# Kernel optimization log

Hardware: AMD Instinct MI355X
Metric: run time of the kernel (lower is better)

## Reference

```python
import jax, jax.numpy as jnp
import numpy as np

B = 131072    # batch of toy 2D points
H = 256       # effective hidden width (dims[1], = out_dims * group_card)
NB = 8        # n_blocks i-ResBlocks
NMID = 3      # middle layers: dims 2->256->256->256->256->2 => 1 in + 3 mid + 1 out
NPS = 5       # n_power_series terms for log-det trace estimator


def setup_inputs() -> dict:
    key = jax.random.key(0)
    ks = jax.random.split(key, 8)
    # small scales keep each g-net contractive (coeff<1 Lipschitz, as spectral norm would)
    x  = jax.random.normal(ks[0], (B, 2), jnp.float32)
    v  = jax.random.normal(ks[1], (B, 2), jnp.float32)  # Hutchinson probe (n_samples=1)
    Wi = jax.random.normal(ks[2], (NB, 2, H), jnp.float32) * 0.05
    bi = jax.random.normal(ks[3], (NB, H), jnp.float32) * 0.01
    Wm = jax.random.normal(ks[4], (NB, NMID, H, H), jnp.float32) * (0.05 / np.sqrt(H))
    bm = jax.random.normal(ks[5], (NB, NMID, H), jnp.float32) * 0.01
    Wo = jax.random.normal(ks[6], (NB, H, 2), jnp.float32) * (0.05 / np.sqrt(H))
    bo = jax.random.normal(ks[7], (NB, 2), jnp.float32) * 0.01
    return {"x": x, "v": v, "Wi": Wi, "bi": bi, "Wm": Wm, "bm": bm, "Wo": Wo, "bo": bo}


def _g(x, Wi, bi, Wm, bm, Wo, bo):
    # equivariant 3x3 convs on 1x1 spatial maps == channel-mixing linears;
    # build_nnet appends the activation after EVERY conv, including the last.
    h = jax.nn.relu(x @ Wi + bi)
    for j in range(Wm.shape[0]):
        h = jax.nn.relu(h @ Wm[j] + bm[j])
    return jax.nn.relu(h @ Wo + bo)


def _iresblock(x, v, Wi, bi, Wm, bm, Wo, bo):
    gfun = lambda xx: _g(xx, Wi, bi, Wm, bm, Wo, bo)
    gx = gfun(x)
    # log det(I + J_g) ~= sum_{k=1..n} (-1)^{k+1}/k * v^T J_g^k v  (power series, Hutchinson)
    w = v
    logdet = jnp.zeros((x.shape[0], 1), x.dtype)
    for k in range(1, NPS + 1):
        _, w = jax.jvp(gfun, (x,), (w,))          # w <- J_g @ w
        coef = ((-1.0) ** (k + 1)) / k
        logdet = logdet + coef * jnp.sum(w * v, axis=1, keepdims=True)
    return x + gx, logdet


def reference(x, v, Wi, bi, Wm, bm, Wo, bo):
    z = x
    delta_logp = jnp.zeros((x.shape[0], 1), x.dtype)  # SequentialFlow: logpx - logdet per block
    for b in range(NB):
        z, ld = _iresblock(z, v, Wi[b], bi[b], Wm[b], bm[b], Wo[b], bo[b])
        delta_logp = delta_logp - ld
    return z, delta_logp
```

## Files before the change

kernel.cpp:

```cpp
#include <hip/hip_runtime.h>
#include <hip/hip_bf16.h>

#define BATCH 131072
#define H 256
#define NBLK 8
#define NMID 3
#define MS 32
#define RT_N 6
#define NT 256

typedef __attribute__((ext_vector_type(8))) short short8;
typedef __attribute__((ext_vector_type(4))) float f32x4;

__device__ __forceinline__ unsigned pk2(float a, float b) {
    unsigned ua = __float_as_uint(a) + 0x8000u;
    unsigned ub = __float_as_uint(b) + 0x8000u;
    return __builtin_amdgcn_perm(ub, ua, 0x07060302u);
}
__device__ __forceinline__ unsigned short f2bf(float f) {
    return (unsigned short)((__float_as_uint(f) + 0x8000u) >> 16);
}

__global__ void pack_w_kernel(const float* __restrict__ Wm, unsigned short* __restrict__ Wp) {
    int o = blockIdx.x * blockDim.x + threadIdx.x;
    if (o >= NBLK * NMID * 8192) return;
    int lane  = o & 63;
    int T     = (o >> 6) & 15;
    int kk    = (o >> 10) & 7;
    int layer = o >> 13;
    int n  = (T >> 2) * 64 + (lane & 15) * 4 + (T & 3);
    int k0 = kk * 32 + (lane >> 4) * 8;
    const float* src = Wm + (size_t)layer * H * H;
    unsigned int w[4];
    #pragma unroll
    for (int jj = 0; jj < 4; ++jj)
        w[jj] = pk2(src[(size_t)(k0 + 2*jj) * H + n], src[(size_t)(k0 + 2*jj + 1) * H + n]);
    uint4 val; val.x = w[0]; val.y = w[1]; val.z = w[2]; val.w = w[3];
    ((uint4*)Wp)[o] = val;
}

__device__ __forceinline__ void epilogue_write(const f32x4 (&acc)[RT_N][4],
                                               const float* __restrict__ bias,
                                               unsigned short* __restrict__ Xs,
                                               int wave, int lane) {
    const int mcol = lane & 15, quad = lane >> 4;
    const int nb = wave * 64 + mcol * 4;
    const float4 bv = *(const float4*)(bias + nb);
    const int kkx = nb >> 5;
    const int qx  = (nb >> 3) & 3;
    const int jb  = nb & 7;
    #pragma unroll
    for (int g = 0; g < 2; ++g) {
        #pragma unroll
        for (int r = 0; r < 4; ++r) {
            float pre[4], hv[4], ta[4], tb[4];
            pre[0] = acc[g][0][r] + bv.x; pre[1] = acc[g][1][r] + bv.y;
            pre[2] = acc[g][2][r] + bv.z; pre[3] = acc[g][3][r] + bv.w;
            #pragma unroll
            for (int c = 0; c < 4; ++c) {
                bool mk = pre[c] > 0.0f;
                hv[c] = mk ? pre[c]        : 0.0f;
                ta[c] = mk ? acc[2+g][c][r] : 0.0f;
                tb[c] = mk ? acc[4+g][c][r] : 0.0f;
            }
            int rowm = quad * 4 + r;
            int le   = qx * 16 + rowm;
            int scl  = le ^ ((le >> 3) & 7);
            int e0   = (((g * 8 + kkx) * 64 + scl) * 8) + jb;
            uint2 ph; ph.x = pk2(hv[0], hv[1]); ph.y = pk2(hv[2], hv[3]);
            uint2 pa; pa.x = pk2(ta[0], ta[1]); pa.y = pk2(ta[2], ta[3]);
            uint2 pb; pb.x = pk2(tb[0], tb[1]); pb.y = pk2(tb[2], tb[3]);
            *(uint2*)(Xs + e0)          = ph;
            *(uint2*)(Xs + e0 + 8192)   = pa;
            *(uint2*)(Xs + e0 + 16384)  = pb;
        }
    }
}

__global__ __launch_bounds__(NT, 2)
void flow_kernel(const float* __restrict__ x, const float* __restrict__ v,
                 const float* __restrict__ Wi, const float* __restrict__ bi,
                 const float* __restrict__ bm, const float* __restrict__ Wo,
                 const float* __restrict__ bo,
                 const unsigned short* __restrict__ Wp,
                 float* __restrict__ out)
{
    __shared__ uint4 Xl4[RT_N * 8 * 64];
    __shared__ float zbuf[MS * 2];
    __shared__ float vbuf[MS * 2];

    unsigned short* Xs = (unsigned short*)Xl4;

    const int tid  = threadIdx.x;
    const int wave = tid >> 6;
    const int lane = tid & 63;
    const int mcol = lane & 15;
    const int quad = lane >> 4;
    const int s0   = blockIdx.x * MS;
    const int rl   = lane ^ ((lane >> 3) & 7);

    float dlp = 0.0f;
    if (tid < MS) {
        zbuf[tid*2+0] = x[(size_t)(s0+tid)*2+0];
        zbuf[tid*2+1] = x[(size_t)(s0+tid)*2+1];
        vbuf[tid*2+0] = v[(size_t)(s0+tid)*2+0];
        vbuf[tid*2+1] = v[(size_t)(s0+tid)*2+1];
    }
    __syncthreads();

    for (int b = 0; b < NBLK; ++b) {
        #pragma unroll
        for (int cc = 0; cc < 2; ++cc) {
            int c = cc * NT + tid;
            if (c < 384) {
                int rt = c >> 6, cl = c & 63;
                int l = cl ^ ((cl >> 3) & 7);
                int m = l & 15, q = l >> 4;
                int st = rt >> 1;
                uint4 pk = {0u, 0u, 0u, 0u};
                if (q == 0) {
                    if (st == 0) {
                        int s = ((rt & 1) << 4) | m;
                        pk.x = pk2(zbuf[s*2+0], zbuf[s*2+1]);
                    } else if (st == 1) pk.x = 0x00003F80u;
                    else                pk.x = 0x3F800000u;
                }
                Xl4[rt * 512 + cl] = pk;
            }
        }
        __syncthreads();

        const float* Wi0 = Wi + (size_t)b * 2 * H;
        const float* Wi1 = Wi0 + H;
        {
            short8 b0[4];
            #pragma unroll
            for (int ct = 0; ct < 4; ++ct) {
                short8 z = {0,0,0,0,0,0,0,0};
                if (lane < 16) {
                    int n = wave * 64 + lane * 4 + ct;
                    unsigned p = pk2(Wi0[n], Wi1[n]);
                    z[0] = (short)(p & 0xFFFFu);
                    z[1] = (short)(p >> 16);
                }
                b0[ct] = z;
            }
            f32x4 acc[RT_N][4];
            #pragma unroll
            for (int rt = 0; rt < RT_N; ++rt)
                #pragma unroll
                for (int ct = 0; ct < 4; ++ct)
                    acc[rt][ct] = (f32x4){0.f, 0.f, 0.f, 0.f};
            #pragma unroll
            for (int rt = 0; rt < RT_N; ++rt) {
                short8 af = ((const short8*)Xl4)[(rt * 8) * 64 + rl];
                #pragma unroll
                for (int ct = 0; ct < 4; ++ct)
                    acc[rt][ct] = __builtin_amdgcn_mfma_f32_16x16x32_bf16(af, b0[ct], acc[rt][ct], 0, 0, 0);
            }
            __syncthreads();
            epilogue_write(acc, bi + (size_t)b * H, Xs, wave, lane);
            __syncthreads();
        }

        for (int li = 0; li < NMID; ++li) {
            const int layer = b * NMID + li;
            const short8* Bp  = ((const short8*)Wp) + (size_t)layer * 8192;
            const float* bias = bm + (size_t)layer * H;

            f32x4 acc[RT_N][4];
            #pragma unroll
            for (int rt = 0; rt < RT_N; ++rt)
                #pragma unroll
                for (int ct = 0; ct < 4; ++ct)
                    acc[rt][ct] = (f32x4){0.f, 0.f, 0.f, 0.f};

            #pragma unroll
            for (int kk = 0; kk < 8; ++kk) {
                short8 bf[4];
                #pragma unroll
                for (int ct = 0; ct < 4; ++ct)
                    bf[ct] = Bp[(kk*16 + wave*4 + ct)*64 + lane];
                #pragma unroll
                for (int rt = 0; rt < RT_N; ++rt) {
                    short8 af = ((const short8*)Xl4)[(rt*8 + kk)*64 + rl];
                    #pragma unroll
                    for (int ct = 0; ct < 4; ++ct)
                        acc[rt][ct] = __builtin_amdgcn_mfma_f32_16x16x32_bf16(af, bf[ct], acc[rt][ct], 0, 0, 0);
                }
            }
            __syncthreads();
            epilogue_write(acc, bias, Xs, wave, lane);
            __syncthreads();
        }

        const float* Wob = Wo + (size_t)b * H * 2;
        const float* bob = bo + (size_t)b * 2;
        {
            short8 b4[2];
            #pragma unroll
            for (int kki = 0; kki < 2; ++kki) {
                short8 z = {0,0,0,0,0,0,0,0};
                if (mcol < 2) {
                    int kb = (wave * 2 + kki) * 32 + quad * 8;
                    #pragma unroll
                    for (int jj = 0; jj < 4; ++jj) {
                        unsigned p = pk2(Wob[(kb + 2*jj) * 2 + mcol], Wob[(kb + 2*jj + 1) * 2 + mcol]);
                        z[2*jj]   = (short)(p & 0xFFFFu);
                        z[2*jj+1] = (short)(p >> 16);
                    }
                }
                b4[kki] = z;
            }
            f32x4 accL[RT_N];
            #pragma unroll
            for (int rt = 0; rt < RT_N; ++rt) accL[rt] = (f32x4){0.f, 0.f, 0.f, 0.f};
            #pragma unroll
            for (int rt = 0; rt < RT_N; ++rt) {
                short8 a0 = ((const short8*)Xl4)[(rt*8 + wave*2    )*64 + rl];
                accL[rt] = __builtin_amdgcn_mfma_f32_16x16x32_bf16(a0, b4[0], accL[rt], 0, 0, 0);
                short8 a1 = ((const short8*)Xl4)[(rt*8 + wave*2 + 1)*64 + rl];
                accL[rt] = __builtin_amdgcn_mfma_f32_16x16x32_bf16(a1, b4[1], accL[rt], 0, 0, 0);
            }
            __syncthreads();
            float* part = (float*)Xl4;
            if (mcol < 2) {
                #pragma unroll
                for (int rt = 0; rt < RT_N; ++rt)
                    #pragma unroll
                    for (int r = 0; r < 4; ++r)
                        part[((rt*16 + quad*4 + r)*2 + mcol)*4 + wave] = accL[rt][r];
            }
            __syncthreads();
            float* res = part + 768;
            if (tid < 192) {
                float4 p4 = ((const float4*)part)[tid];
                res[tid] = p4.x + p4.y + p4.z + p4.w;
            }
            __syncthreads();
            if (tid < MS) {
                int g = tid >> 4, row = tid & 15;
                int base = (g * 16 + row) * 2;
                float SH0 = res[base], SH1 = res[base + 1];
                float SA0 = res[base + 64], SA1 = res[base + 65];
                float SB0 = res[base + 128], SB1 = res[base + 129];
                float pre0 = SH0 + bob[0], pre1 = SH1 + bob[1];
                bool  m0 = pre0 > 0.f,     m1 = pre1 > 0.f;
                float gx0 = m0 ? pre0 : 0.f, gx1 = m1 ? pre1 : 0.f;
                float J00 = m0 ? SA0 : 0.f;
                float J01 = m0 ? SB0 : 0.f;
                float J10 = m1 ? SA1 : 0.f;
                float J11 = m1 ? SB1 : 0.f;
                float v0 = vbuf[tid*2+0], v1 = vbuf[tid*2+1];
                float w0 = v0, w1 = v1, ld = 0.f;
                const float coef[5] = {1.f, -0.5f, 1.f/3.f, -0.25f, 0.2f};
                #pragma unroll
                for (int k = 0; k < 5; ++k) {
                    float nw0 = fmaf(J00, w0, J01 * w1);
                    float nw1 = fmaf(J10, w0, J11 * w1);
                    w0 = nw0; w1 = nw1;
                    ld = fmaf(coef[k], fmaf(w0, v0, w1 * v1), ld);
                }
                zbuf[tid*2+0] += gx0;
                zbuf[tid*2+1] += gx1;
                dlp -= ld;
            }
        }
        __syncthreads();
    }

    if (tid < MS) {
        out[(size_t)(s0+tid)*2+0] = zbuf[tid*2+0];
        out[(size_t)(s0+tid)*2+1] = zbuf[tid*2+1];
        out[(size_t)2*BATCH + s0 + tid] = dlp;
    }
}

extern "C" void kernel_launch(void* const* d_in, const int* in_sizes, int n_in,
                              void* d_out, int out_size, void* d_ws, size_t ws_size,
                              hipStream_t stream) {
    const float* x  = (const float*)d_in[0];
    const float* v  = (const float*)d_in[1];
    const float* Wi = (const float*)d_in[2];
    const float* bi = (const float*)d_in[3];
    const float* Wm = (const float*)d_in[4];
    const float* bm = (const float*)d_in[5];
    const float* Wo = (const float*)d_in[6];
    const float* bo = (const float*)d_in[7];
    unsigned short* Wp = (unsigned short*)d_ws;

    int nchunks = NBLK * NMID * 8192;
    pack_w_kernel<<<(nchunks + 255) / 256, 256, 0, stream>>>(Wm, Wp);
    flow_kernel<<<BATCH / MS, NT, 0, stream>>>(x, v, Wi, bi, bm, Wo, bo, Wp, (float*)d_out);
}
```

Measured before the change: 1.253 ms.

## Split output columns across eight waves per block instead of four

Doubles the block to 512 threads (8 waves) and has each wave own half as many output column tiles in every layer, which halves the accumulator registers per wave. Launch bounds change to allow 4 blocks per CU, and the middle-layer k-loop unroll drops to 2. The output-layer reduction now sums eight per-wave partials. The aim is more resident waves to hide LDS and global weight-load latency. The cost is that each A fragment loaded from LDS feeds only half as many MFMAs, so LDS traffic per unit of compute doubles, and barriers now span more waves.

```diff
diff --git a/kernel.cpp b/kernel.cpp
--- a/kernel.cpp
+++ b/kernel.cpp
@@ -7,7 +7,7 @@
 #define NMID 3
 #define MS 32
 #define RT_N 6
-#define NT 256
+#define NT 512
 
 typedef __attribute__((ext_vector_type(8))) short short8;
 typedef __attribute__((ext_vector_type(4))) float f32x4;
@@ -16,9 +16,6 @@
     unsigned ua = __float_as_uint(a) + 0x8000u;
     unsigned ub = __float_as_uint(b) + 0x8000u;
     return __builtin_amdgcn_perm(ub, ua, 0x07060302u);
-}
-__device__ __forceinline__ unsigned short f2bf(float f) {
-    return (unsigned short)((__float_as_uint(f) + 0x8000u) >> 16);
 }
 
 __global__ void pack_w_kernel(const float* __restrict__ Wm, unsigned short* __restrict__ Wp) {
@@ -39,45 +36,38 @@
     ((uint4*)Wp)[o] = val;
 }
 
-__device__ __forceinline__ void epilogue_write(const f32x4 (&acc)[RT_N][4],
+__device__ __forceinline__ void epilogue_write(const f32x4 (&acc)[RT_N][2],
                                                const float* __restrict__ bias,
                                                unsigned short* __restrict__ Xs,
                                                int wave, int lane) {
     const int mcol = lane & 15, quad = lane >> 4;
-    const int nb = wave * 64 + mcol * 4;
-    const float4 bv = *(const float4*)(bias + nb);
-    const int kkx = nb >> 5;
-    const int qx  = (nb >> 3) & 3;
-    const int jb  = nb & 7;
+    const int C  = (wave >> 1) * 64 + mcol * 4 + ((wave & 1) << 1);
+    const float b0 = bias[C], b1 = bias[C + 1];
+    const int kkx = C >> 5;
+    const int qx  = (C >> 3) & 3;
+    const int jb  = C & 7;
     #pragma unroll
     for (int g = 0; g < 2; ++g) {
         #pragma unroll
         for (int r = 0; r < 4; ++r) {
-            float pre[4], hv[4], ta[4], tb[4];
-            pre[0] = acc[g][0][r] + bv.x; pre[1] = acc[g][1][r] + bv.y;
-            pre[2] = acc[g][2][r] + bv.z; pre[3] = acc[g][3][r] + bv.w;
-            #pragma unroll
-            for (int c = 0; c < 4; ++c) {
-                bool mk = pre[c] > 0.0f;
-                hv[c] = mk ? pre[c]        : 0.0f;
-                ta[c] = mk ? acc[2+g][c][r] : 0.0f;
-                tb[c] = mk ? acc[4+g][c][r] : 0.0f;
-            }
+            float pre0 = acc[g][0][r] + b0;
+            float pre1 = acc[g][1][r] + b1;
+            bool m0 = pre0 > 0.0f, m1 = pre1 > 0.0f;
+            float h0 = m0 ? pre0 : 0.0f,          h1 = m1 ? pre1 : 0.0f;
+            float a0 = m0 ? acc[2+g][0][r] : 0.0f, a1 = m1 ? acc[2+g][1][r] : 0.0f;
+            float t0 = m0 ? acc[4+g][0][r] : 0.0f, t1 = m1 ? acc[4+g][1][r] : 0.0f;
             int rowm = quad * 4 + r;
             int le   = qx * 16 + rowm;
             int scl  = le ^ ((le >> 3) & 7);
             int e0   = (((g * 8 + kkx) * 64 + scl) * 8) + jb;
-            uint2 ph; ph.x = pk2(hv[0], hv[1]); ph.y = pk2(hv[2], hv[3]);
-            uint2 pa; pa.x = pk2(ta[0], ta[1]); pa.y = pk2(ta[2], ta[3]);
-            uint2 pb; pb.x = pk2(tb[0], tb[1]); pb.y = pk2(tb[2], tb[3]);
-            *(uint2*)(Xs + e0)          = ph;
-            *(uint2*)(Xs + e0 + 8192)   = pa;
-            *(uint2*)(Xs + e0 + 16384)  = pb;
-        }
-    }
-}
-
-__global__ __launch_bounds__(NT, 2)
+            *(unsigned*)(Xs + e0)          = pk2(h0, h1);
+            *(unsigned*)(Xs + e0 + 8192)   = pk2(a0, a1);
+            *(unsigned*)(Xs + e0 + 16384)  = pk2(t0, t1);
+        }
+    }
+}
+
+__global__ __launch_bounds__(NT, 4)
 void flow_kernel(const float* __restrict__ x, const float* __restrict__ v,
                  const float* __restrict__ Wi, const float* __restrict__ bi,
                  const float* __restrict__ bm, const float* __restrict__ Wo,
@@ -109,54 +99,50 @@
     __syncthreads();
 
     for (int b = 0; b < NBLK; ++b) {
-        #pragma unroll
-        for (int cc = 0; cc < 2; ++cc) {
-            int c = cc * NT + tid;
-            if (c < 384) {
-                int rt = c >> 6, cl = c & 63;
-                int l = cl ^ ((cl >> 3) & 7);
-                int m = l & 15, q = l >> 4;
-                int st = rt >> 1;
-                uint4 pk = {0u, 0u, 0u, 0u};
-                if (q == 0) {
-                    if (st == 0) {
-                        int s = ((rt & 1) << 4) | m;
-                        pk.x = pk2(zbuf[s*2+0], zbuf[s*2+1]);
-                    } else if (st == 1) pk.x = 0x00003F80u;
-                    else                pk.x = 0x3F800000u;
-                }
-                Xl4[rt * 512 + cl] = pk;
-            }
+        if (tid < 384) {
+            int rt = tid >> 6, cl = tid & 63;
+            int l = cl ^ ((cl >> 3) & 7);
+            int m = l & 15, q = l >> 4;
+            int st = rt >> 1;
+            uint4 pk = {0u, 0u, 0u, 0u};
+            if (q == 0) {
+                if (st == 0) {
+                    int s = ((rt & 1) << 4) | m;
+                    pk.x = pk2(zbuf[s*2+0], zbuf[s*2+1]);
+                } else if (st == 1) pk.x = 0x00003F80u;
+                else                pk.x = 0x3F800000u;
+            }
+            Xl4[rt * 512 + cl] = pk;
         }
         __syncthreads();
 
         const float* Wi0 = Wi + (size_t)b * 2 * H;
         const float* Wi1 = Wi0 + H;
         {
-            short8 b0[4];
-            #pragma unroll
-            for (int ct = 0; ct < 4; ++ct) {
+            short8 b0f[2];
+            #pragma unroll
+            for (int ct = 0; ct < 2; ++ct) {
                 short8 z = {0,0,0,0,0,0,0,0};
                 if (lane < 16) {
-                    int n = wave * 64 + lane * 4 + ct;
+                    int n = (wave >> 1) * 64 + lane * 4 + ((wave & 1) << 1) + ct;
                     unsigned p = pk2(Wi0[n], Wi1[n]);
                     z[0] = (short)(p & 0xFFFFu);
                     z[1] = (short)(p >> 16);
                 }
-                b0[ct] = z;
-            }
-            f32x4 acc[RT_N][4];
+                b0f[ct] = z;
+            }
+            f32x4 acc[RT_N][2];
             #pragma unroll
             for (int rt = 0; rt < RT_N; ++rt)
                 #pragma unroll
-                for (int ct = 0; ct < 4; ++ct)
+                for (int ct = 0; ct < 2; ++ct)
                     acc[rt][ct] = (f32x4){0.f, 0.f, 0.f, 0.f};
             #pragma unroll
             for (int rt = 0; rt < RT_N; ++rt) {
                 short8 af = ((const short8*)Xl4)[(rt * 8) * 64 + rl];
                 #pragma unroll
-                for (int ct = 0; ct < 4; ++ct)
-                    acc[rt][ct] = __builtin_amdgcn_mfma_f32_16x16x32_bf16(af, b0[ct], acc[rt][ct], 0, 0, 0);
+                for (int ct = 0; ct < 2; ++ct)
+                    acc[rt][ct] = __builtin_amdgcn_mfma_f32_16x16x32_bf16(af, b0f[ct], acc[rt][ct], 0, 0, 0);
             }
             __syncthreads();
             epilogue_write(acc, bi + (size_t)b * H, Xs, wave, lane);
@@ -168,24 +154,24 @@
             const short8* Bp  = ((const short8*)Wp) + (size_t)layer * 8192;
             const float* bias = bm + (size_t)layer * H;
 
-            f32x4 acc[RT_N][4];
+            f32x4 acc[RT_N][2];
             #pragma unroll
             for (int rt = 0; rt < RT_N; ++rt)
                 #pragma unroll
-                for (int ct = 0; ct < 4; ++ct)
+                for (int ct = 0; ct < 2; ++ct)
                     acc[rt][ct] = (f32x4){0.f, 0.f, 0.f, 0.f};
 
-            #pragma unroll
+            #pragma unroll 2
             for (int kk = 0; kk < 8; ++kk) {
-                short8 bf[4];
-                #pragma unroll
-                for (int ct = 0; ct < 4; ++ct)
-                    bf[ct] = Bp[(kk*16 + wave*4 + ct)*64 + lane];
+                short8 bf[2];
+                #pragma unroll
+                for (int ct = 0; ct < 2; ++ct)
+                    bf[ct] = Bp[(kk*16 + wave*2 + ct)*64 + lane];
                 #pragma unroll
                 for (int rt = 0; rt < RT_N; ++rt) {
                     short8 af = ((const short8*)Xl4)[(rt*8 + kk)*64 + rl];
                     #pragma unroll
-                    for (int ct = 0; ct < 4; ++ct)
+                    for (int ct = 0; ct < 2; ++ct)
                         acc[rt][ct] = __builtin_amdgcn_mfma_f32_16x16x32_bf16(af, bf[ct], acc[rt][ct], 0, 0, 0);
                 }
             }
@@ -197,30 +183,23 @@
         const float* Wob = Wo + (size_t)b * H * 2;
         const float* bob = bo + (size_t)b * 2;
         {
-            short8 b4[2];
-            #pragma unroll
-            for (int kki = 0; kki < 2; ++kki) {
-                short8 z = {0,0,0,0,0,0,0,0};
-                if (mcol < 2) {
-                    int kb = (wave * 2 + kki) * 32 + quad * 8;
-                    #pragma unroll
-                    for (int jj = 0; jj < 4; ++jj) {
-                        unsigned p = pk2(Wob[(kb + 2*jj) * 2 + mcol], Wob[(kb + 2*jj + 1) * 2 + mcol]);
-                        z[2*jj]   = (short)(p & 0xFFFFu);
-                        z[2*jj+1] = (short)(p >> 16);
-                    }
-                }
-                b4[kki] = z;
+            short8 b4 = {0,0,0,0,0,0,0,0};
+            if (mcol < 2) {
+                int kb = wave * 32 + quad * 8;
+                #pragma unroll
+                for (int jj = 0; jj < 4; ++jj) {
+                    unsigned p = pk2(Wob[(kb + 2*jj) * 2 + mcol], Wob[(kb + 2*jj + 1) * 2 + mcol]);
+                    b4[2*jj]   = (short)(p & 0xFFFFu);
+                    b4[2*jj+1] = (short)(p >> 16);
+                }
             }
             f32x4 accL[RT_N];
             #pragma unroll
             for (int rt = 0; rt < RT_N; ++rt) accL[rt] = (f32x4){0.f, 0.f, 0.f, 0.f};
             #pragma unroll
             for (int rt = 0; rt < RT_N; ++rt) {
-                short8 a0 = ((const short8*)Xl4)[(rt*8 + wave*2    )*64 + rl];
-                accL[rt] = __builtin_amdgcn_mfma_f32_16x16x32_bf16(a0, b4[0], accL[rt], 0, 0, 0);
-                short8 a1 = ((const short8*)Xl4)[(rt*8 + wave*2 + 1)*64 + rl];
-                accL[rt] = __builtin_amdgcn_mfma_f32_16x16x32_bf16(a1, b4[1], accL[rt], 0, 0, 0);
+                short8 a0 = ((const short8*)Xl4)[(rt*8 + wave)*64 + rl];
+                accL[rt] = __builtin_amdgcn_mfma_f32_16x16x32_bf16(a0, b4, accL[rt], 0, 0, 0);
             }
             __syncthreads();
             float* part = (float*)Xl4;
@@ -229,13 +208,14 @@
                 for (int rt = 0; rt < RT_N; ++rt)
                     #pragma unroll
                     for (int r = 0; r < 4; ++r)
-                        part[((rt*16 + quad*4 + r)*2 + mcol)*4 + wave] = accL[rt][r];
-            }
-            __syncthreads();
-            float* res = part + 768;
+                        part[((rt*16 + quad*4 + r)*2 + mcol)*8 + wave] = accL[rt][r];
+            }
+            __syncthreads();
+            float* res = part + 1536;
             if (tid < 192) {
-                float4 p4 = ((const float4*)part)[tid];
-                res[tid] = p4.x + p4.y + p4.z + p4.w;
+                float4 p4 = ((const float4*)part)[tid*2];
+                float4 q4 = ((const float4*)part)[tid*2 + 1];
+                res[tid] = (p4.x + p4.y + p4.z + p4.w) + (q4.x + q4.y + q4.z + q4.w);
             }
             __syncthreads();
             if (tid < MS) {
```

Result: faster. 1.195 ms (-4.6%).
